# Kernel tuning notes

Hardware: AMD Instinct MI355X
Metric: run time of the kernel (lower is better)

Reference implementation:

```python
import jax, jax.numpy as jnp
import numpy as np

L, D, HID, NH, E, K, P, IMG, NC, B = 4, 384, 1536, 6, 8, 2, 16, 224, 1000, 8
S = (IMG // P) ** 2 + 1  # 197 tokens (cls + patches)
EPS = 1e-5


def setup_inputs() -> dict:
    ks = iter(jax.random.split(jax.random.key(0), 32))
    g = lambda shape, s=0.02: jax.random.normal(next(ks), shape, jnp.float32) * s
    pd = 3 * P * P
    return dict(
        x=jax.random.normal(next(ks), (B, 3, IMG, IMG), jnp.float32),
        patch_w=g((pd, D)), patch_b=g((D,)),
        cls_tok=g((1, 1, D)), pos=g((1, S, D)),
        qkv_w=g((L, D, 3 * D)), qkv_b=g((L, 3 * D)),
        proj_w=g((L, D, D)), proj_b=g((L, D)),
        ln1_g=jnp.ones((L, D)), ln1_b=jnp.zeros((L, D)),
        ln2_g=jnp.ones((L, D)), ln2_b=jnp.zeros((L, D)),
        router_w=g((L, D, E)), router_b=g((L, E)),
        w1=g((L, E, D, HID)), b1=g((L, E, HID)),
        w2=g((L, E, HID, D)), b2=g((L, E, D)),
        norm_g=jnp.ones((D,)), norm_b=jnp.zeros((D,)),
        fc_w=g((D, NC)), fc_b=g((NC,)),
    )


def _ln(x, g, b):
    m = x.mean(-1, keepdims=True)
    v = ((x - m) ** 2).mean(-1, keepdims=True)
    return (x - m) * jax.lax.rsqrt(v + EPS) * g + b


def _mha(x, wqkv, bqkv, wo, bo):
    Bx, Sx, Dx = x.shape
    hd = Dx // NH
    qkv = x @ wqkv + bqkv
    q, k, v = jnp.split(qkv, 3, axis=-1)
    q = q.reshape(Bx, Sx, NH, hd)
    k = k.reshape(Bx, Sx, NH, hd)
    v = v.reshape(Bx, Sx, NH, hd)
    att = jnp.einsum('bqhd,bkhd->bhqk', q, k) / jnp.sqrt(jnp.float32(hd))
    att = jax.nn.softmax(att, axis=-1)
    o = jnp.einsum('bhqk,bkhd->bqhd', att, v).reshape(Bx, Sx, Dx)
    return o @ wo + bo


def _moe(x, rw, rb, w1, b1, w2, b2, noise):
    # Faithful to the masked-dense SparseMoE: non-routed experts see zeros,
    # so occupied experts leak expert_j(0)=gelu(b1_j)@W2_j+b2_j to all tokens.
    xf = x.reshape(-1, x.shape[-1])                     # [T, D]
    logits = xf @ rw + rb + noise * 0.01                # noisy gating
    vals, idx = jax.lax.top_k(logits, K)                # [T, K]
    gates = jax.nn.softmax(vals, axis=-1)               # [T, K]
    h = jax.nn.gelu(jnp.einsum('td,edh->teh', xf, w1) + b1[None], approximate=False)
    y = jnp.einsum('teh,ehd->ted', h, w2) + b2[None]    # [T, E, D]
    bias0 = jnp.einsum('eh,ehd->ed', jax.nn.gelu(b1, approximate=False), w2) + b2  # expert_j(0)
    oh = jax.nn.one_hot(idx, E, dtype=xf.dtype)         # [T, K, E]
    occ = (oh.sum(0) > 0).astype(xf.dtype)              # [K, E] slot occupancy (mask.sum()>0)
    bias_sum = occ @ bias0                              # [K, D]
    y_sel = jnp.take_along_axis(y, idx[:, :, None], axis=1)  # [T, K, D]
    out = jnp.einsum('tk,tkd->td', gates, y_sel - bias0[idx] + bias_sum[None])
    return out.reshape(x.shape)


def reference(x, patch_w, patch_b, cls_tok, pos, qkv_w, qkv_b, proj_w, proj_b,
              ln1_g, ln1_b, ln2_g, ln2_b, router_w, router_b,
              w1, b1, w2, b2, norm_g, norm_b, fc_w, fc_b):
    Bx = x.shape[0]
    Hp = IMG // P
    # torch unfold patchify: (B,C,Hp,Wp,p,p) -> (B, N, C*p*p), channel-major features
    patches = x.reshape(Bx, 3, Hp, P, Hp, P).transpose(0, 2, 4, 1, 3, 5).reshape(Bx, Hp * Hp, 3 * P * P)
    t = patches @ patch_w + patch_b
    t = jnp.concatenate([jnp.broadcast_to(cls_tok, (Bx, 1, D)), t], axis=1) + pos
    nkey = jax.random.key(42)
    for l in range(L):
        a = _mha(t, qkv_w[l], qkv_b[l], proj_w[l], proj_b[l])
        t = _ln(t + a, ln1_g[l], ln1_b[l])
        noise = jax.random.normal(jax.random.fold_in(nkey, l), (Bx * S, E), t.dtype)
        m = _moe(t, router_w[l], router_b[l], w1[l], b1[l], w2[l], b2[l], noise)
        t = _ln(t + m, ln2_g[l], ln2_b[l])
    t = _ln(t, norm_g, norm_b)
    return t[:, 0] @ fc_w + fc_b
```

## Files before the change

### kernel.cpp

```cpp
#include <hip/hip_runtime.h>
#include <hip/hip_bf16.h>

constexpr int LYR  = 4;
constexpr int DM   = 384;
constexpr int HIDN = 1536;
constexpr int NHEAD = 6;
constexpr int HDIM = 64;
constexpr int NEXP = 8;
constexpr int SEQ  = 197;
constexpr int BATCH = 8;
constexpr int TOK  = BATCH * SEQ;
constexpr int NCLS = 1000;
constexpr int CAPE = TOK;
constexpr int NPATCH = BATCH * 196;
constexpr float EPSLN = 1e-5f;
constexpr int KP = 40;

typedef __attribute__((ext_vector_type(8))) short short8v;
typedef __attribute__((ext_vector_type(4))) float f32x4v;

__host__ __device__ inline void tf2x32(unsigned k0, unsigned k1, unsigned x0, unsigned x1,
                                       unsigned& y0, unsigned& y1) {
  unsigned ks2 = k0 ^ k1 ^ 0x1BD11BDAu;
  unsigned v0 = x0 + k0, v1 = x1 + k1;
#define TFR(r) { v0 += v1; v1 = (v1 << (r)) | (v1 >> (32 - (r))); v1 ^= v0; }
  TFR(13) TFR(15) TFR(26) TFR(6)
  v0 += k1;  v1 += ks2 + 1u;
  TFR(17) TFR(29) TFR(16) TFR(24)
  v0 += ks2; v1 += k0 + 2u;
  TFR(13) TFR(15) TFR(26) TFR(6)
  v0 += k0;  v1 += k1 + 3u;
  TFR(17) TFR(29) TFR(16) TFR(24)
  v0 += k1;  v1 += ks2 + 4u;
  TFR(13) TFR(15) TFR(26) TFR(6)
  v0 += ks2; v1 += k0 + 5u;
#undef TFR
  y0 = v0; y1 = v1;
}

__device__ inline float erfinv32(float x) {
  float w = -log1pf(-x * x);
  float p;
  if (w < 5.f) {
    w -= 2.5f;
    p = 2.81022636e-08f;
    p = fmaf(p, w, 3.43273939e-07f);
    p = fmaf(p, w, -3.5233877e-06f);
    p = fmaf(p, w, -4.39150654e-06f);
    p = fmaf(p, w, 0.00021858087f);
    p = fmaf(p, w, -0.00125372503f);
    p = fmaf(p, w, -0.00417768164f);
    p = fmaf(p, w, 0.246640727f);
    p = fmaf(p, w, 1.50140941f);
  } else {
    w = sqrtf(w) - 3.f;
    p = -0.000200214257f;
    p = fmaf(p, w, 0.000100950558f);
    p = fmaf(p, w, 0.00134934322f);
    p = fmaf(p, w, -0.00367342844f);
    p = fmaf(p, w, 0.00573950773f);
    p = fmaf(p, w, -0.0076224613f);
    p = fmaf(p, w, 0.00943887047f);
    p = fmaf(p, w, 1.00167406f);
    p = fmaf(p, w, 2.83297682f);
  }
  return p * x;
}

__device__ inline float gelu_f(float x) {
  return 0.5f * x * (1.f + erff(x * 0.70710678118654752f));
}

__device__ inline unsigned short bf16_rne(float x) {
  unsigned u = __float_as_uint(x);
  unsigned r = (u + 0x7fffu + ((u >> 16) & 1u)) >> 16;
  return (unsigned short)r;
}
__device__ inline void split2(float x, short& hs, short& ls) {
  unsigned hu = bf16_rne(x);
  float hf = __uint_as_float(hu << 16);
  unsigned lu = bf16_rne(x - hf);
  hs = (short)hu; ls = (short)lu;
}

__global__ __launch_bounds__(256) void convw_kernel(const float* __restrict__ src,
                                                    short* __restrict__ dst,
                                                    int K, int N) {
  const int nchunks = (K >> 5) * (N >> 4);
  const int chunk = blockIdx.x * 4 + (threadIdx.x >> 6);
  if (chunk >= nchunks) return;
  const int lane = threadIdx.x & 63;
  const long eoffS = (long)blockIdx.y * K * N;
  const long eoffD = (long)blockIdx.y * nchunks * 1024;
  const int nc = N >> 4;
  const int kt = chunk / nc, nt = chunk - kt * nc;
  const int n = nt * 16 + (lane & 15);
  const int kb = kt * 32 + (lane >> 4) * 8;
  short8v hv, lv;
#pragma unroll
  for (int j = 0; j < 8; j++) {
    short h, l;
    split2(src[eoffS + (long)(kb + j) * N + n], h, l);
    hv[j] = h; lv[j] = l;
  }
  *(short8v*)&dst[eoffD + (long)chunk * 1024 + lane * 8] = hv;
  *(short8v*)&dst[eoffD + (long)chunk * 1024 + 512 + lane * 8] = lv;
}

template <int KTOT, int NTOT, int MODE>
__global__ __launch_bounds__(256) void mfma_gemm_kernel(const float* __restrict__ A,
                                                        const short* __restrict__ Wf,
                                                        const float* __restrict__ bias,
                                                        const int* __restrict__ lists,
                                                        const int* __restrict__ counts,
                                                        float* __restrict__ out) {
  const int e = MODE ? blockIdx.y : 0;
  int rowsM;
  if (MODE) {
    const int n = counts[e];
    if ((int)blockIdx.x * 64 >= n) return;
    rowsM = min(64, n - (int)blockIdx.x * 64);
  } else {
    rowsM = min(64, TOK - (int)blockIdx.x * 64);
  }
  const int c0 = blockIdx.z * 64;
  const int tid = threadIdx.x;
  const int w = tid >> 6, lane = tid & 63;
  __shared__ int ent[64];
  __shared__ short xh[64 * KP];
  __shared__ short xl[64 * KP];
  if (MODE) {
    if (tid < 64) ent[tid] = (tid < rowsM) ? lists[e * CAPE + blockIdx.x * 64 + tid] : -1;
    __syncthreads();
  }
  const int sr = tid >> 2, skq = (tid & 3) * 8;
  bool okr; long arow = 0;
  if (MODE == 0) {
    okr = (sr < rowsM);
    arow = (long)(blockIdx.x * 64 + sr) * KTOT;
  } else {
    const int pid = ent[sr];
    okr = (pid >= 0);
    arow = (long)((MODE == 1) ? (pid >> 1) : pid) * KTOT;
  }
  const short* W = Wf + (long)e * (KTOT >> 5) * (NTOT >> 4) * 1024;
  const int wm = (w >> 1) * 32, wn = (w & 1) * 32;
  f32x4v Cr[2][2] = {};
  float4 ra = make_float4(0.f, 0.f, 0.f, 0.f), rb = ra;
  if (okr) {
    ra = *(const float4*)&A[arow + skq];
    rb = *(const float4*)&A[arow + skq + 4];
  }
  for (int kt = 0; kt < KTOT / 32; ++kt) {
    __syncthreads();
    {
      const float v[8] = {ra.x, ra.y, ra.z, ra.w, rb.x, rb.y, rb.z, rb.w};
      short8v hv, lv;
#pragma unroll
      for (int j = 0; j < 8; j++) { short h, l; split2(v[j], h, l); hv[j] = h; lv[j] = l; }
      *(short8v*)&xh[sr * KP + skq] = hv;
      *(short8v*)&xl[sr * KP + skq] = lv;
    }
    if (kt + 1 < KTOT / 32 && okr) {
      ra = *(const float4*)&A[arow + (kt + 1) * 32 + skq];
      rb = *(const float4*)&A[arow + (kt + 1) * 32 + skq + 4];
    }
    __syncthreads();
    short8v bhv[2], blv[2];
#pragma unroll
    for (int tt = 0; tt < 2; ++tt) {
      const int trow = wm + tt * 16 + (lane & 15);
      bhv[tt] = *(const short8v*)&xh[trow * KP + (lane >> 4) * 8];
      blv[tt] = *(const short8v*)&xl[trow * KP + (lane >> 4) * 8];
    }
    const long wkb = ((long)kt * (NTOT >> 4) + (c0 >> 4) + (wn >> 4)) * 1024;
#pragma unroll
    for (int nt = 0; nt < 2; ++nt) {
      const short8v wh = *(const short8v*)&W[wkb + nt * 1024 + lane * 8];
      const short8v wl = *(const short8v*)&W[wkb + nt * 1024 + 512 + lane * 8];
#pragma unroll
      for (int tt = 0; tt < 2; ++tt) {
        Cr[tt][nt] = __builtin_amdgcn_mfma_f32_16x16x32_bf16(wh, bhv[tt], Cr[tt][nt], 0, 0, 0);
        Cr[tt][nt] = __builtin_amdgcn_mfma_f32_16x16x32_bf16(wh, blv[tt], Cr[tt][nt], 0, 0, 0);
        Cr[tt][nt] = __builtin_amdgcn_mfma_f32_16x16x32_bf16(wl, bhv[tt], Cr[tt][nt], 0, 0, 0);
      }
    }
  }
  const int tl = lane & 15;
  const int nq = (lane >> 4) * 4;
#pragma unroll
  for (int tt = 0; tt < 2; ++tt) {
    const int trow = wm + tt * 16 + tl;
    if (trow < rowsM) {
      long orow;
      if (MODE == 0) orow = (long)(blockIdx.x * 64 + trow) * NTOT;
      else orow = (long)ent[trow] * NTOT;
#pragma unroll
      for (int nt = 0; nt < 2; ++nt) {
        const int n = c0 + wn + nt * 16 + nq;
        const float4 bv = *(const float4*)&bias[(MODE ? e * NTOT : 0) + n];
        float4 o;
        o.x = Cr[tt][nt][0] + bv.x;
        o.y = Cr[tt][nt][1] + bv.y;
        o.z = Cr[tt][nt][2] + bv.z;
        o.w = Cr[tt][nt][3] + bv.w;
        if (MODE == 1) { o.x = gelu_f(o.x); o.y = gelu_f(o.y); o.z = gelu_f(o.z); o.w = gelu_f(o.w); }
        *(float4*)&out[orow + n] = o;
      }
    }
  }
}

__global__ __launch_bounds__(256) void patch_mfma_kernel(const float* __restrict__ x,
                                                         const short* __restrict__ Wf,
                                                         const float* __restrict__ pb,
                                                         const float* __restrict__ pos,
                                                         float* __restrict__ t) {
  constexpr int KTOT = 768, NTOT = DM;
  const int rowsM = min(64, NPATCH - (int)blockIdx.x * 64);
  const int c0 = blockIdx.z * 64;
  const int tid = threadIdx.x;
  const int w = tid >> 6, lane = tid & 63;
  __shared__ short xh[64 * KP];
  __shared__ short xl[64 * KP];
  const int sr = tid >> 2, skq = (tid & 3) * 8;
  const bool okr = (sr < rowsM);
  const int p = blockIdx.x * 64 + sr;
  const int pbat = okr ? (p / 196) : 0;
  const int pn = okr ? (p - pbat * 196) : 0;
  const int hp = pn / 14, wp = pn - hp * 14;
  const float* xbase = x + ((long)pbat * 3 * 224 + hp * 16) * 224 + wp * 16;
  const int wm = (w >> 1) * 32, wn = (w & 1) * 32;
  f32x4v Cr[2][2] = {};
  float4 ra = make_float4(0.f, 0.f, 0.f, 0.f), rb = ra;
  if (okr) {
    const int f = skq;
    const int c = f >> 8, py = (f >> 4) & 15, px = f & 15;
    const float* ptr = xbase + ((long)c * 224 + py) * 224 + px;
    ra = *(const float4*)ptr;
    rb = *(const float4*)(ptr + 4);
  }
  for (int kt = 0; kt < KTOT / 32; ++kt) {
    __syncthreads();
    {
      const float v[8] = {ra.x, ra.y, ra.z, ra.w, rb.x, rb.y, rb.z, rb.w};
      short8v hv, lv;
#pragma unroll
      for (int j = 0; j < 8; j++) { short h, l; split2(v[j], h, l); hv[j] = h; lv[j] = l; }
      *(short8v*)&xh[sr * KP + skq] = hv;
      *(short8v*)&xl[sr * KP + skq] = lv;
    }
    if (kt + 1 < KTOT / 32 && okr) {
      const int f = (kt + 1) * 32 + skq;
      const int c = f >> 8, py = (f >> 4) & 15, px = f & 15;
      const float* ptr = xbase + ((long)c * 224 + py) * 224 + px;
      ra = *(const float4*)ptr;
      rb = *(const float4*)(ptr + 4);
    }
    __syncthreads();
    short8v bhv[2], blv[2];
#pragma unroll
    for (int tt = 0; tt < 2; ++tt) {
      const int trow = wm + tt * 16 + (lane & 15);
      bhv[tt] = *(const short8v*)&xh[trow * KP + (lane >> 4) * 8];
      blv[tt] = *(const short8v*)&xl[trow * KP + (lane >> 4) * 8];
    }
    const long wkb = ((long)kt * (NTOT >> 4) + (c0 >> 4) + (wn >> 4)) * 1024;
#pragma unroll
    for (int nt = 0; nt < 2; ++nt) {
      const short8v wh = *(const short8v*)&Wf[wkb + nt * 1024 + lane * 8];
      const short8v wl = *(const short8v*)&Wf[wkb + nt * 1024 + 512 + lane * 8];
#pragma unroll
      for (int tt = 0; tt < 2; ++tt) {
        Cr[tt][nt] = __builtin_amdgcn_mfma_f32_16x16x32_bf16(wh, bhv[tt], Cr[tt][nt], 0, 0, 0);
        Cr[tt][nt] = __builtin_amdgcn_mfma_f32_16x16x32_bf16(wh, blv[tt], Cr[tt][nt], 0, 0, 0);
        Cr[tt][nt] = __builtin_amdgcn_mfma_f32_16x16x32_bf16(wl, bhv[tt], Cr[tt][nt], 0, 0, 0);
      }
    }
  }
  const int tl = lane & 15;
  const int nq = (lane >> 4) * 4;
#pragma unroll
  for (int tt = 0; tt < 2; ++tt) {
    const int trow = wm + tt * 16 + tl;
    if (trow < rowsM) {
      const int r = blockIdx.x * 64 + trow;
      const int b2 = r / 196, n2 = r - b2 * 196;
      const long orow = (long)(b2 * SEQ + 1 + n2) * DM;
#pragma unroll
      for (int nt = 0; nt < 2; ++nt) {
        const int n = c0 + wn + nt * 16 + nq;
        const float4 bv = *(const float4*)&pb[n];
        const float4 pv = *(const float4*)&pos[(1 + n2) * DM + n];
        float4 o;
        o.x = Cr[tt][nt][0] + bv.x + pv.x;
        o.y = Cr[tt][nt][1] + bv.y + pv.y;
        o.z = Cr[tt][nt][2] + bv.z + pv.z;
        o.w = Cr[tt][nt][3] + bv.w + pv.w;
        *(float4*)&t[orow + n] = o;
      }
    }
  }
}

__global__ void cls_pos_kernel(const float* __restrict__ cls, const float* __restrict__ pos,
                               float* __restrict__ t) {
  int b = blockIdx.x, d = threadIdx.x;
  t[(b * SEQ) * DM + d] = cls[d] + pos[d];
}

constexpr int QT = 32;
constexpr int SP = 208;
__global__ __launch_bounds__(256) void attn_tile_kernel(const float* __restrict__ qkv,
                                                        float* __restrict__ out) {
  const int bh = blockIdx.x;
  const int b = bh / NHEAD, h = bh % NHEAD;
  const int q0 = blockIdx.y * QT;
  const int nq = min(QT, SEQ - q0);
  __shared__ float Qs[64][QT + 4];
  __shared__ float KV[64][68];
  __shared__ float Ss[QT][SP];
  const int tid = threadIdx.x;
  const int tx = tid & 15, ty = tid >> 4;
  for (int i = tid; i < QT * 16; i += 256) {
    const int q = i >> 4, dq = (i & 15) << 2;
    float4 v = make_float4(0.f, 0.f, 0.f, 0.f);
    if (q < nq) v = *(const float4*)&qkv[(long)(b * SEQ + q0 + q) * 1152 + h * HDIM + dq];
    Qs[dq + 0][q] = v.x; Qs[dq + 1][q] = v.y; Qs[dq + 2][q] = v.z; Qs[dq + 3][q] = v.w;
  }
  for (int kt = 0; kt < 4; ++kt) {
    const int kbase = kt * 64;
    __syncthreads();
    for (int i = tid; i < 64 * 16; i += 256) {
      const int key = i >> 4, dq = (i & 15) << 2;
      float4 v = make_float4(0.f, 0.f, 0.f, 0.f);
      if (kbase + key < SEQ)
        v = *(const float4*)&qkv[(long)(b * SEQ + kbase + key) * 1152 + DM + h * HDIM + dq];
      KV[dq + 0][key] = v.x; KV[dq + 1][key] = v.y; KV[dq + 2][key] = v.z; KV[dq + 3][key] = v.w;
    }
    __syncthreads();
    float acc[2][4] = {};
#pragma unroll 16
    for (int d = 0; d < 64; ++d) {
      const float4 k4 = *(const float4*)&KV[d][tx << 2];
      const float a0 = Qs[d][ty * 2], a1 = Qs[d][ty * 2 + 1];
      const float kk[4] = {k4.x, k4.y, k4.z, k4.w};
#pragma unroll
      for (int j = 0; j < 4; j++) {
        acc[0][j] = fmaf(a0, kk[j], acc[0][j]);
        acc[1][j] = fmaf(a1, kk[j], acc[1][j]);
      }
    }
#pragma unroll
    for (int i = 0; i < 2; i++) {
      float4 o = make_float4(acc[i][0] * 0.125f, acc[i][1] * 0.125f,
                             acc[i][2] * 0.125f, acc[i][3] * 0.125f);
      *(float4*)&Ss[ty * 2 + i][kbase + (tx << 2)] = o;
    }
  }
  __syncthreads();
  {
    const int row = tid >> 3, c = tid & 7;
    float m = -1e30f;
    for (int k = c; k < SEQ; k += 8) m = fmaxf(m, Ss[row][k]);
    m = fmaxf(m, __shfl_xor(m, 1)); m = fmaxf(m, __shfl_xor(m, 2)); m = fmaxf(m, __shfl_xor(m, 4));
    float s = 0.f;
    for (int k = c; k < SEQ; k += 8) { float e2 = __expf(Ss[row][k] - m); Ss[row][k] = e2; s += e2; }
    s += __shfl_xor(s, 1); s += __shfl_xor(s, 2); s += __shfl_xor(s, 4);
    const float inv = 1.f / s;
    for (int k = c; k < SEQ; k += 8) Ss[row][k] *= inv;
  }
  float acc[2][4] = {};
  for (int kt = 0; kt < 4; ++kt) {
    const int kbase = kt * 64;
    const int kend = min(64, SEQ - kbase);
    __syncthreads();
    for (int i = tid; i < 64 * 16; i += 256) {
      const int key = i >> 4, dq = (i & 15) << 2;
      float4 v = make_float4(0.f, 0.f, 0.f, 0.f);
      if (kbase + key < SEQ)
        v = *(const float4*)&qkv[(long)(b * SEQ + kbase + key) * 1152 + 2 * DM + h * HDIM + dq];
      *(float4*)&KV[key][dq] = v;
    }
    __syncthreads();
    for (int k = 0; k < kend; ++k) {
      const float4 v4 = *(const float4*)&KV[k][tx << 2];
      const float p0 = Ss[ty * 2][kbase + k], p1 = Ss[ty * 2 + 1][kbase + k];
      const float vv[4] = {v4.x, v4.y, v4.z, v4.w};
#pragma unroll
      for (int j = 0; j < 4; j++) {
        acc[0][j] = fmaf(p0, vv[j], acc[0][j]);
        acc[1][j] = fmaf(p1, vv[j], acc[1][j]);
      }
    }
  }
#pragma unroll
  for (int i = 0; i < 2; i++) {
    const int row = ty * 2 + i;
    if (row < nq) {
      float4 o = make_float4(acc[i][0], acc[i][1], acc[i][2], acc[i][3]);
      *(float4*)&out[(long)(b * SEQ + q0 + row) * DM + h * HDIM + (tx << 2)] = o;
    }
  }
}

__global__ __launch_bounds__(384) void add_ln_kernel(float* __restrict__ t,
                                                     const float* __restrict__ delta,
                                                     const float* __restrict__ g,
                                                     const float* __restrict__ bta) {
  int tok = blockIdx.x, d = threadIdx.x;
  float v = t[tok * DM + d] + delta[tok * DM + d];
  float sv = v, sq = v * v;
  for (int off = 32; off > 0; off >>= 1) { sv += __shfl_xor(sv, off); sq += __shfl_xor(sq, off); }
  __shared__ float rs[6], rq[6];
  int w = d >> 6, ln = d & 63;
  if (ln == 0) { rs[w] = sv; rq[w] = sq; }
  __syncthreads();
  float mean = 0.f, ms = 0.f;
#pragma unroll
  for (int i = 0; i < 6; i++) { mean += rs[i]; ms += rq[i]; }
  mean *= (1.f / DM); ms *= (1.f / DM);
  float inv = rsqrtf(ms - mean * mean + EPSLN);
  t[tok * DM + d] = (v - mean) * inv * g[d] + bta[d];
}

__global__ __launch_bounds__(256) void router_logits_kernel(const float* __restrict__ t,
                                                            const float* __restrict__ rw,
                                                            const float* __restrict__ rb,
                                                            unsigned k0, unsigned k1,
                                                            float* __restrict__ gates,
                                                            int* __restrict__ idxb) {
  const int tok = blockIdx.x * 4 + (threadIdx.x >> 6);
  const int lane = threadIdx.x & 63;
  const int e = lane & 7, j = lane >> 3;
  const float* xr = t + tok * DM;
  float acc = 0.f;
  for (int d2 = j * 48; d2 < j * 48 + 48; d2++) acc += xr[d2] * rw[d2 * NEXP + e];
  acc += __shfl_xor(acc, 8);
  acc += __shfl_xor(acc, 16);
  acc += __shfl_xor(acc, 32);
  if (lane < 8) {
    acc += rb[e];
    unsigned i = (unsigned)(tok * NEXP + e);
    unsigned y0, y1;
    tf2x32(k0, k1, 0u, i, y0, y1);
    unsigned bits = y0 ^ y1;
    float f = __uint_as_float(0x3f800000u | (bits >> 9)) - 1.0f;
    const float lo = -0.99999994f;
    float u = f * 2.0f + lo;
    u = fmaxf(lo, u);
    acc += 0.01f * (1.41421356f * erfinv32(u));
  }
  float lg[8];
#pragma unroll
  for (int qq = 0; qq < 8; qq++) lg[qq] = __shfl(acc, qq);
  if (lane == 0) {
    int i0 = 0; float v0 = lg[0];
#pragma unroll
    for (int qq = 1; qq < 8; qq++) if (lg[qq] > v0) { v0 = lg[qq]; i0 = qq; }
    int i1 = -1; float v1 = -1e30f;
#pragma unroll
    for (int qq = 0; qq < 8; qq++) if (qq != i0 && lg[qq] > v1) { v1 = lg[qq]; i1 = qq; }
    float e1 = __expf(v1 - v0);
    float g0 = 1.f / (1.f + e1);
    idxb[tok * 2] = i0; idxb[tok * 2 + 1] = i1;
    gates[tok * 2] = g0; gates[tok * 2 + 1] = 1.f - g0;
  }
}

__global__ __launch_bounds__(1024) void bucket_kernel(const int* __restrict__ idxb,
                                                      int* __restrict__ lists,
                                                      int* __restrict__ counts,
                                                      int* __restrict__ occ) {
  __shared__ int lc[NEXP];
  __shared__ int locc[2 * NEXP];
  const int tid = threadIdx.x;
  if (tid < NEXP) lc[tid] = 0;
  if (tid < 2 * NEXP) locc[tid] = 0;
  __syncthreads();
  for (int i = tid; i < 2 * TOK; i += 1024) {
    const int e = idxb[i];
    const int p = atomicAdd(&lc[e], 1);
    lists[e * CAPE + p] = i;
    locc[(i & 1) * NEXP + e] = 1;
  }
  __syncthreads();
  if (tid < NEXP) counts[tid] = lc[tid];
  if (tid < 2 * NEXP) occ[tid] = locc[tid];
}

__global__ void prep_kernel(const float* __restrict__ b2, float* __restrict__ bias0) {
  int e = blockIdx.x, c = threadIdx.x;
  bias0[e * DM + c] = b2[e * DM + c];
}

__global__ __launch_bounds__(384) void bias0_partial_kernel(const float* __restrict__ b1,
                                                            const float* __restrict__ w2,
                                                            float* __restrict__ bias0) {
  const int e = blockIdx.x, kc = blockIdx.y;
  __shared__ float gb[128];
  const int tid = threadIdx.x;
  if (tid < 128) gb[tid] = gelu_f(b1[e * HIDN + kc * 128 + tid]);
  __syncthreads();
  float acc = 0.f;
  const float* W = w2 + ((long)e * HIDN + kc * 128) * DM + tid;
  for (int j2 = 0; j2 < 128; j2++) acc += gb[j2] * W[(long)j2 * DM];
  atomicAdd(&bias0[e * DM + tid], acc);
}

__global__ __launch_bounds__(384) void bias_sum_kernel(const float* __restrict__ bias0,
                                                       const int* __restrict__ occ,
                                                       float* __restrict__ bias_sum) {
  int k = blockIdx.x, d = threadIdx.x;
  float acc = 0.f;
#pragma unroll
  for (int e = 0; e < NEXP; e++)
    if (occ[k * NEXP + e]) acc += bias0[e * DM + d];
  bias_sum[k * DM + d] = acc;
}

__global__ __launch_bounds__(384) void moe_combine_ln_kernel(float* __restrict__ t,
                                                             const float* __restrict__ ybuf,
                                                             const float* __restrict__ gates,
                                                             const int* __restrict__ idxb,
                                                             const float* __restrict__ bias0,
                                                             const float* __restrict__ bias_sum,
                                                             const float* __restrict__ g,
                                                             const float* __restrict__ bta) {
  int tok = blockIdx.x, d = threadIdx.x;
  float g0 = gates[tok * 2], g1 = gates[tok * 2 + 1];
  int i0 = idxb[tok * 2], i1 = idxb[tok * 2 + 1];
  float m0 = ybuf[(tok * 2) * DM + d] - bias0[i0 * DM + d] + bias_sum[d];
  float m1 = ybuf[(tok * 2 + 1) * DM + d] - bias0[i1 * DM + d] + bias_sum[DM + d];
  float v = t[tok * DM + d] + g0 * m0 + g1 * m1;
  float sv = v, sq = v * v;
  for (int off = 32; off > 0; off >>= 1) { sv += __shfl_xor(sv, off); sq += __shfl_xor(sq, off); }
  __shared__ float rs[6], rq[6];
  int w = d >> 6, ln = d & 63;
  if (ln == 0) { rs[w] = sv; rq[w] = sq; }
  __syncthreads();
  float mean = 0.f, ms = 0.f;
#pragma unroll
  for (int i = 0; i < 6; i++) { mean += rs[i]; ms += rq[i]; }
  mean *= (1.f / DM); ms *= (1.f / DM);
  float inv = rsqrtf(ms - mean * mean + EPSLN);
  t[tok * DM + d] = (v - mean) * inv * g[d] + bta[d];
}

__global__ __launch_bounds__(256) void final_kernel(const float* __restrict__ t,
                                                    const float* __restrict__ ng,
                                                    const float* __restrict__ nb,
                                                    const float* __restrict__ fw,
                                                    const float* __restrict__ fb,
                                                    float* __restrict__ out) {
  int b = blockIdx.x, chunk = blockIdx.y, tid = threadIdx.x;
  __shared__ float xr[DM];
  __shared__ float rs[4], rq[4];
  const float* row = t + (b * SEQ) * DM;
  float sv = 0.f, sq = 0.f;
  for (int i = tid; i < DM; i += 256) { float x = row[i]; xr[i] = x; sv += x; sq += x * x; }
  for (int off = 32; off > 0; off >>= 1) { sv += __shfl_xor(sv, off); sq += __shfl_xor(sq, off); }
  int w = tid >> 6, ln = tid & 63;
  if (ln == 0) { rs[w] = sv; rq[w] = sq; }
  __syncthreads();
  float mean = (rs[0] + rs[1] + rs[2] + rs[3]) * (1.f / DM);
  float ms = (rq[0] + rq[1] + rq[2] + rq[3]) * (1.f / DM);
  float inv = rsqrtf(ms - mean * mean + EPSLN);
  for (int i = tid; i < DM; i += 256) xr[i] = (xr[i] - mean) * inv * ng[i] + nb[i];
  __syncthreads();
  int c = chunk * 250 + tid;
  if (tid < 250) {
    float acc = fb[c];
    for (int k = 0; k < DM; k++) acc += xr[k] * fw[k * NCLS + c];
    out[b * NCLS + c] = acc;
  }
}

extern "C" void kernel_launch(void* const* d_in, const int* in_sizes, int n_in,
                              void* d_out, int out_size, void* d_ws, size_t ws_size,
                              hipStream_t stream) {
  const float* x       = (const float*)d_in[0];
  const float* patch_w = (const float*)d_in[1];
  const float* patch_b = (const float*)d_in[2];
  const float* cls_tok = (const float*)d_in[3];
  const float* pos     = (const float*)d_in[4];
  const float* qkv_w   = (const float*)d_in[5];
  const float* qkv_b   = (const float*)d_in[6];
  const float* proj_w  = (const float*)d_in[7];
  const float* proj_b  = (const float*)d_in[8];
  const float* ln1_g   = (const float*)d_in[9];
  const float* ln1_b   = (const float*)d_in[10];
  const float* ln2_g   = (const float*)d_in[11];
  const float* ln2_b   = (const float*)d_in[12];
  const float* router_w = (const float*)d_in[13];
  const float* router_b = (const float*)d_in[14];
  const float* w1      = (const float*)d_in[15];
  const float* b1      = (const float*)d_in[16];
  const float* w2      = (const float*)d_in[17];
  const float* b2      = (const float*)d_in[18];
  const float* norm_g  = (const float*)d_in[19];
  const float* norm_b  = (const float*)d_in[20];
  const float* fc_w    = (const float*)d_in[21];
  const float* fc_b    = (const float*)d_in[22];

  float* ws = (float*)d_ws;
  float* t        = ws;
  float* qkv      = t + TOK * DM;
  float* attn     = qkv + TOK * 1152;
  float* proj     = attn + TOK * DM;
  float* ybuf     = proj + TOK * DM;
  float* bias0    = ybuf + TOK * 2 * DM;
  float* bias_sum = bias0 + NEXP * DM;
  float* gates    = bias_sum + 2 * DM;
  int* idxb   = (int*)(gates + TOK * 2);
  int* lists  = idxb + TOK * 2;
  int* counts = lists + NEXP * CAPE;
  int* occ    = counts + NEXP;
  float* hbuf = (float*)(occ + 2 * NEXP);
  short* wqf  = (short*)(hbuf + 2 * TOK * HIDN);
  short* wpf  = wqf + 864 * 1024;
  short* w1f  = wpf + 288 * 1024;
  short* w2f  = w1f + 8 * 1152 * 1024;
  short* wpatf = w2f + 8 * 1152 * 1024;

  convw_kernel<<<dim3(144, 1), 256, 0, stream>>>(patch_w, wpatf, 768, DM);
  patch_mfma_kernel<<<dim3(25, 1, 6), 256, 0, stream>>>(x, wpatf, patch_b, pos, t);
  cls_pos_kernel<<<BATCH, DM, 0, stream>>>(cls_tok, pos, t);

  for (int l = 0; l < LYR; l++) {
    convw_kernel<<<dim3(216, 1), 256, 0, stream>>>(qkv_w + (long)l * DM * 1152, wqf, DM, 1152);
    convw_kernel<<<dim3(72, 1), 256, 0, stream>>>(proj_w + (long)l * DM * DM, wpf, DM, DM);
    convw_kernel<<<dim3(288, NEXP), 256, 0, stream>>>(w1 + (long)l * NEXP * DM * HIDN, w1f, DM, HIDN);
    convw_kernel<<<dim3(288, NEXP), 256, 0, stream>>>(w2 + (long)l * NEXP * HIDN * DM, w2f, HIDN, DM);

    mfma_gemm_kernel<DM, 1152, 0><<<dim3(25, 1, 18), 256, 0, stream>>>(
        t, wqf, qkv_b + l * 1152, nullptr, nullptr, qkv);
    attn_tile_kernel<<<dim3(BATCH * NHEAD, 7), 256, 0, stream>>>(qkv, attn);
    mfma_gemm_kernel<DM, DM, 0><<<dim3(25, 1, 6), 256, 0, stream>>>(
        attn, wpf, proj_b + l * DM, nullptr, nullptr, proj);
    add_ln_kernel<<<TOK, DM, 0, stream>>>(t, proj, ln1_g + l * DM, ln1_b + l * DM);

    prep_kernel<<<NEXP, DM, 0, stream>>>(b2 + l * NEXP * DM, bias0);
    bias0_partial_kernel<<<dim3(NEXP, 12), 384, 0, stream>>>(
        b1 + l * NEXP * HIDN, w2 + (long)l * NEXP * HIDN * DM, bias0);
    unsigned kl0, kl1;
    tf2x32(0u, 42u, 0u, (unsigned)l, kl0, kl1);
    router_logits_kernel<<<TOK / 4, 256, 0, stream>>>(
        t, router_w + l * DM * NEXP, router_b + l * NEXP, kl0, kl1, gates, idxb);
    bucket_kernel<<<1, 1024, 0, stream>>>(idxb, lists, counts, occ);
    bias_sum_kernel<<<2, 384, 0, stream>>>(bias0, occ, bias_sum);
    mfma_gemm_kernel<DM, HIDN, 1><<<dim3(25, NEXP, 24), 256, 0, stream>>>(
        t, w1f, b1 + l * NEXP * HIDN, lists, counts, hbuf);
    mfma_gemm_kernel<HIDN, DM, 2><<<dim3(25, NEXP, 6), 256, 0, stream>>>(
        hbuf, w2f, b2 + l * NEXP * DM, lists, counts, ybuf);
    moe_combine_ln_kernel<<<TOK, DM, 0, stream>>>(t, ybuf, gates, idxb, bias0, bias_sum,
                                                  ln2_g + l * DM, ln2_b + l * DM);
  }

  final_kernel<<<dim3(BATCH, 4), 256, 0, stream>>>(t, norm_g, norm_b, fc_w, fc_b,
                                                   (float*)d_out);
}
```

Baseline: 913.7 us.

## Pre-split activations into bf16 hi/lo planes in producers; GEMMs load fragments directly

Producer kernels (patch embed, cls, attention, add-LN, combine-LN, expert FFN1 epilogue) now also write activations as bf16 hi/lo split planes. The GEMMs read these straight from global memory into MFMA fragments, dropping the per-tile LDS staging, the in-loop fp32 split and both barriers. The grid is also reordered so column strips come first, which may improve weight reuse in cache. In exchange the producers write extra short buffers, and A-fragment loads are uncoalesced direct global reads.

```diff
diff --git a/kernel.cpp b/kernel.cpp
--- a/kernel.cpp
+++ b/kernel.cpp
@@ -17,6 +17,7 @@
 constexpr int KP = 40;
 
 typedef __attribute__((ext_vector_type(8))) short short8v;
+typedef __attribute__((ext_vector_type(4))) short short4v;
 typedef __attribute__((ext_vector_type(4))) float f32x4v;
 
 __host__ __device__ inline void tf2x32(unsigned k0, unsigned k1, unsigned x0, unsigned x1,
@@ -108,70 +109,47 @@
 }
 
 template <int KTOT, int NTOT, int MODE>
-__global__ __launch_bounds__(256) void mfma_gemm_kernel(const float* __restrict__ A,
-                                                        const short* __restrict__ Wf,
-                                                        const float* __restrict__ bias,
-                                                        const int* __restrict__ lists,
-                                                        const int* __restrict__ counts,
-                                                        float* __restrict__ out) {
-  const int e = MODE ? blockIdx.y : 0;
-  int rowsM;
-  if (MODE) {
-    const int n = counts[e];
-    if ((int)blockIdx.x * 64 >= n) return;
-    rowsM = min(64, n - (int)blockIdx.x * 64);
-  } else {
-    rowsM = min(64, TOK - (int)blockIdx.x * 64);
-  }
-  const int c0 = blockIdx.z * 64;
+__global__ __launch_bounds__(256) void gemm_frag_kernel(
+    const short* __restrict__ Ah, const short* __restrict__ Al,
+    const short* __restrict__ Wf, const float* __restrict__ bias,
+    const int* __restrict__ lists, const int* __restrict__ counts,
+    float* __restrict__ outF, short* __restrict__ outH, short* __restrict__ outL) {
+  constexpr int SPE = NTOT / 64;
+  const int strip = blockIdx.x;
+  const int e = MODE ? (strip / SPE) : 0;
+  const int c0 = (MODE ? (strip - e * SPE) : strip) * 64;
+  const int m = blockIdx.y;
+  int cnt = TOK;
+  if (MODE) cnt = counts[e];
+  if (m * 64 >= cnt) return;
   const int tid = threadIdx.x;
   const int w = tid >> 6, lane = tid & 63;
-  __shared__ int ent[64];
-  __shared__ short xh[64 * KP];
-  __shared__ short xl[64 * KP];
-  if (MODE) {
-    if (tid < 64) ent[tid] = (tid < rowsM) ? lists[e * CAPE + blockIdx.x * 64 + tid] : -1;
-    __syncthreads();
-  }
-  const int sr = tid >> 2, skq = (tid & 3) * 8;
-  bool okr; long arow = 0;
-  if (MODE == 0) {
-    okr = (sr < rowsM);
-    arow = (long)(blockIdx.x * 64 + sr) * KTOT;
-  } else {
-    const int pid = ent[sr];
-    okr = (pid >= 0);
-    arow = (long)((MODE == 1) ? (pid >> 1) : pid) * KTOT;
-  }
-  const short* W = Wf + (long)e * (KTOT >> 5) * (NTOT >> 4) * 1024;
   const int wm = (w >> 1) * 32, wn = (w & 1) * 32;
+  const int tl = lane & 15, kq = (lane >> 4) * 8;
+  int pid[2]; long arow[2];
+#pragma unroll
+  for (int tt = 0; tt < 2; ++tt) {
+    const int r = m * 64 + wm + tt * 16 + tl;
+    int p;
+    if (MODE) {
+      p = (r < cnt) ? lists[e * CAPE + r] : -1;
+      const int rr = (p < 0) ? 0 : ((MODE == 1) ? (p >> 1) : p);
+      arow[tt] = (long)rr * KTOT;
+    } else {
+      p = (r < TOK) ? r : -1;
+      arow[tt] = (long)((p < 0) ? 0 : r) * KTOT;
+    }
+    pid[tt] = p;
+  }
+  const short* W = Wf + (long)e * ((KTOT >> 5) * (NTOT >> 4)) * 1024;
   f32x4v Cr[2][2] = {};
-  float4 ra = make_float4(0.f, 0.f, 0.f, 0.f), rb = ra;
-  if (okr) {
-    ra = *(const float4*)&A[arow + skq];
-    rb = *(const float4*)&A[arow + skq + 4];
-  }
+#pragma unroll 4
   for (int kt = 0; kt < KTOT / 32; ++kt) {
-    __syncthreads();
-    {
-      const float v[8] = {ra.x, ra.y, ra.z, ra.w, rb.x, rb.y, rb.z, rb.w};
-      short8v hv, lv;
-#pragma unroll
-      for (int j = 0; j < 8; j++) { short h, l; split2(v[j], h, l); hv[j] = h; lv[j] = l; }
-      *(short8v*)&xh[sr * KP + skq] = hv;
-      *(short8v*)&xl[sr * KP + skq] = lv;
-    }
-    if (kt + 1 < KTOT / 32 && okr) {
-      ra = *(const float4*)&A[arow + (kt + 1) * 32 + skq];
-      rb = *(const float4*)&A[arow + (kt + 1) * 32 + skq + 4];
-    }
-    __syncthreads();
-    short8v bhv[2], blv[2];
+    short8v bh[2], bl[2];
 #pragma unroll
     for (int tt = 0; tt < 2; ++tt) {
-      const int trow = wm + tt * 16 + (lane & 15);
-      bhv[tt] = *(const short8v*)&xh[trow * KP + (lane >> 4) * 8];
-      blv[tt] = *(const short8v*)&xl[trow * KP + (lane >> 4) * 8];
+      bh[tt] = *(const short8v*)&Ah[arow[tt] + kt * 32 + kq];
+      bl[tt] = *(const short8v*)&Al[arow[tt] + kt * 32 + kq];
     }
     const long wkb = ((long)kt * (NTOT >> 4) + (c0 >> 4) + (wn >> 4)) * 1024;
 #pragma unroll
@@ -180,32 +158,34 @@
       const short8v wl = *(const short8v*)&W[wkb + nt * 1024 + 512 + lane * 8];
 #pragma unroll
       for (int tt = 0; tt < 2; ++tt) {
-        Cr[tt][nt] = __builtin_amdgcn_mfma_f32_16x16x32_bf16(wh, bhv[tt], Cr[tt][nt], 0, 0, 0);
-        Cr[tt][nt] = __builtin_amdgcn_mfma_f32_16x16x32_bf16(wh, blv[tt], Cr[tt][nt], 0, 0, 0);
-        Cr[tt][nt] = __builtin_amdgcn_mfma_f32_16x16x32_bf16(wl, bhv[tt], Cr[tt][nt], 0, 0, 0);
+        Cr[tt][nt] = __builtin_amdgcn_mfma_f32_16x16x32_bf16(wh, bh[tt], Cr[tt][nt], 0, 0, 0);
+        Cr[tt][nt] = __builtin_amdgcn_mfma_f32_16x16x32_bf16(wh, bl[tt], Cr[tt][nt], 0, 0, 0);
+        Cr[tt][nt] = __builtin_amdgcn_mfma_f32_16x16x32_bf16(wl, bh[tt], Cr[tt][nt], 0, 0, 0);
       }
     }
   }
-  const int tl = lane & 15;
   const int nq = (lane >> 4) * 4;
 #pragma unroll
   for (int tt = 0; tt < 2; ++tt) {
-    const int trow = wm + tt * 16 + tl;
-    if (trow < rowsM) {
-      long orow;
-      if (MODE == 0) orow = (long)(blockIdx.x * 64 + trow) * NTOT;
-      else orow = (long)ent[trow] * NTOT;
-#pragma unroll
-      for (int nt = 0; nt < 2; ++nt) {
-        const int n = c0 + wn + nt * 16 + nq;
-        const float4 bv = *(const float4*)&bias[(MODE ? e * NTOT : 0) + n];
-        float4 o;
-        o.x = Cr[tt][nt][0] + bv.x;
-        o.y = Cr[tt][nt][1] + bv.y;
-        o.z = Cr[tt][nt][2] + bv.z;
-        o.w = Cr[tt][nt][3] + bv.w;
-        if (MODE == 1) { o.x = gelu_f(o.x); o.y = gelu_f(o.y); o.z = gelu_f(o.z); o.w = gelu_f(o.w); }
-        *(float4*)&out[orow + n] = o;
+    if (pid[tt] < 0) continue;
+    const long orow = (long)pid[tt] * NTOT;
+#pragma unroll
+    for (int nt = 0; nt < 2; ++nt) {
+      const int n = c0 + wn + nt * 16 + nq;
+      const float4 bv = *(const float4*)&bias[(MODE ? e * NTOT : 0) + n];
+      float o0 = Cr[tt][nt][0] + bv.x, o1 = Cr[tt][nt][1] + bv.y;
+      float o2 = Cr[tt][nt][2] + bv.z, o3 = Cr[tt][nt][3] + bv.w;
+      if (MODE == 1) {
+        o0 = gelu_f(o0); o1 = gelu_f(o1); o2 = gelu_f(o2); o3 = gelu_f(o3);
+        short4v hv, lv; short hs, ls;
+        split2(o0, hs, ls); hv[0] = hs; lv[0] = ls;
+        split2(o1, hs, ls); hv[1] = hs; lv[1] = ls;
+        split2(o2, hs, ls); hv[2] = hs; lv[2] = ls;
+        split2(o3, hs, ls); hv[3] = hs; lv[3] = ls;
+        *(short4v*)&outH[orow + n] = hv;
+        *(short4v*)&outL[orow + n] = lv;
+      } else {
+        *(float4*)&outF[orow + n] = make_float4(o0, o1, o2, o3);
       }
     }
   }
@@ -215,7 +195,9 @@
                                                          const short* __restrict__ Wf,
                                                          const float* __restrict__ pb,
                                                          const float* __restrict__ pos,
-                                                         float* __restrict__ t) {
+                                                         float* __restrict__ t,
+                                                         short* __restrict__ tfh,
+                                                         short* __restrict__ tfl) {
   constexpr int KTOT = 768, NTOT = DM;
   const int rowsM = min(64, NPATCH - (int)blockIdx.x * 64);
   const int c0 = blockIdx.z * 64;
@@ -292,27 +274,39 @@
         const int n = c0 + wn + nt * 16 + nq;
         const float4 bv = *(const float4*)&pb[n];
         const float4 pv = *(const float4*)&pos[(1 + n2) * DM + n];
-        float4 o;
-        o.x = Cr[tt][nt][0] + bv.x + pv.x;
-        o.y = Cr[tt][nt][1] + bv.y + pv.y;
-        o.z = Cr[tt][nt][2] + bv.z + pv.z;
-        o.w = Cr[tt][nt][3] + bv.w + pv.w;
-        *(float4*)&t[orow + n] = o;
+        float o0 = Cr[tt][nt][0] + bv.x + pv.x;
+        float o1 = Cr[tt][nt][1] + bv.y + pv.y;
+        float o2 = Cr[tt][nt][2] + bv.z + pv.z;
+        float o3 = Cr[tt][nt][3] + bv.w + pv.w;
+        *(float4*)&t[orow + n] = make_float4(o0, o1, o2, o3);
+        short4v hv, lv; short hs, ls;
+        split2(o0, hs, ls); hv[0] = hs; lv[0] = ls;
+        split2(o1, hs, ls); hv[1] = hs; lv[1] = ls;
+        split2(o2, hs, ls); hv[2] = hs; lv[2] = ls;
+        split2(o3, hs, ls); hv[3] = hs; lv[3] = ls;
+        *(short4v*)&tfh[orow + n] = hv;
+        *(short4v*)&tfl[orow + n] = lv;
       }
     }
   }
 }
 
 __global__ void cls_pos_kernel(const float* __restrict__ cls, const float* __restrict__ pos,
-                               float* __restrict__ t) {
+                               float* __restrict__ t,
+                               short* __restrict__ tfh, short* __restrict__ tfl) {
   int b = blockIdx.x, d = threadIdx.x;
-  t[(b * SEQ) * DM + d] = cls[d] + pos[d];
+  float v = cls[d] + pos[d];
+  t[(b * SEQ) * DM + d] = v;
+  short hs, ls; split2(v, hs, ls);
+  tfh[(b * SEQ) * DM + d] = hs;
+  tfl[(b * SEQ) * DM + d] = ls;
 }
 
 constexpr int QT = 32;
 constexpr int SP = 208;
 __global__ __launch_bounds__(256) void attn_tile_kernel(const float* __restrict__ qkv,
-                                                        float* __restrict__ out) {
+                                                        short* __restrict__ afh,
+                                                        short* __restrict__ afl) {
   const int bh = blockIdx.x;
   const int b = bh / NHEAD, h = bh % NHEAD;
   const int q0 = blockIdx.y * QT;
@@ -398,8 +392,14 @@
   for (int i = 0; i < 2; i++) {
     const int row = ty * 2 + i;
     if (row < nq) {
-      float4 o = make_float4(acc[i][0], acc[i][1], acc[i][2], acc[i][3]);
-      *(float4*)&out[(long)(b * SEQ + q0 + row) * DM + h * HDIM + (tx << 2)] = o;
+      const long o = (long)(b * SEQ + q0 + row) * DM + h * HDIM + (tx << 2);
+      short4v hv, lv; short hs, ls;
+      split2(acc[i][0], hs, ls); hv[0] = hs; lv[0] = ls;
+      split2(acc[i][1], hs, ls); hv[1] = hs; lv[1] = ls;
+      split2(acc[i][2], hs, ls); hv[2] = hs; lv[2] = ls;
+      split2(acc[i][3], hs, ls); hv[3] = hs; lv[3] = ls;
+      *(short4v*)&afh[o] = hv;
+      *(short4v*)&afl[o] = lv;
     }
   }
 }
@@ -407,7 +407,9 @@
 __global__ __launch_bounds__(384) void add_ln_kernel(float* __restrict__ t,
                                                      const float* __restrict__ delta,
                                                      const float* __restrict__ g,
-                                                     const float* __restrict__ bta) {
+                                                     const float* __restrict__ bta,
+                                                     short* __restrict__ tfh,
+                                                     short* __restrict__ tfl) {
   int tok = blockIdx.x, d = threadIdx.x;
   float v = t[tok * DM + d] + delta[tok * DM + d];
   float sv = v, sq = v * v;
@@ -421,7 +423,11 @@
   for (int i = 0; i < 6; i++) { mean += rs[i]; ms += rq[i]; }
   mean *= (1.f / DM); ms *= (1.f / DM);
   float inv = rsqrtf(ms - mean * mean + EPSLN);
-  t[tok * DM + d] = (v - mean) * inv * g[d] + bta[d];
+  float y = (v - mean) * inv * g[d] + bta[d];
+  t[tok * DM + d] = y;
+  short hs, ls; split2(y, hs, ls);
+  tfh[tok * DM + d] = hs;
+  tfl[tok * DM + d] = ls;
 }
 
 __global__ __launch_bounds__(256) void router_logits_kernel(const float* __restrict__ t,
@@ -526,7 +532,9 @@
                                                              const float* __restrict__ bias0,
                                                              const float* __restrict__ bias_sum,
                                                              const float* __restrict__ g,
-                                                             const float* __restrict__ bta) {
+                                                             const float* __restrict__ bta,
+                                                             short* __restrict__ tfh,
+                                                             short* __restrict__ tfl) {
   int tok = blockIdx.x, d = threadIdx.x;
   float g0 = gates[tok * 2], g1 = gates[tok * 2 + 1];
   int i0 = idxb[tok * 2], i1 = idxb[tok * 2 + 1];
@@ -544,7 +552,11 @@
   for (int i = 0; i < 6; i++) { mean += rs[i]; ms += rq[i]; }
   mean *= (1.f / DM); ms *= (1.f / DM);
   float inv = rsqrtf(ms - mean * mean + EPSLN);
-  t[tok * DM + d] = (v - mean) * inv * g[d] + bta[d];
+  float y = (v - mean) * inv * g[d] + bta[d];
+  t[tok * DM + d] = y;
+  short hs, ls; split2(y, hs, ls);
+  tfh[tok * DM + d] = hs;
+  tfl[tok * DM + d] = ls;
 }
 
 __global__ __launch_bounds__(256) void final_kernel(const float* __restrict__ t,
@@ -606,8 +618,7 @@
   float* ws = (float*)d_ws;
   float* t        = ws;
   float* qkv      = t + TOK * DM;
-  float* attn     = qkv + TOK * 1152;
-  float* proj     = attn + TOK * DM;
+  float* proj     = qkv + TOK * 1152;
   float* ybuf     = proj + TOK * DM;
   float* bias0    = ybuf + TOK * 2 * DM;
   float* bias_sum = bias0 + NEXP * DM;
@@ -616,16 +627,21 @@
   int* lists  = idxb + TOK * 2;
   int* counts = lists + NEXP * CAPE;
   int* occ    = counts + NEXP;
-  float* hbuf = (float*)(occ + 2 * NEXP);
-  short* wqf  = (short*)(hbuf + 2 * TOK * HIDN);
-  short* wpf  = wqf + 864 * 1024;
-  short* w1f  = wpf + 288 * 1024;
-  short* w2f  = w1f + 8 * 1152 * 1024;
+  short* tfh = (short*)(occ + 2 * NEXP);
+  short* tfl = tfh + TOK * DM;
+  short* afh = tfl + TOK * DM;
+  short* afl = afh + TOK * DM;
+  short* hbh = afl + TOK * DM;
+  short* hbl = hbh + 2 * TOK * HIDN;
+  short* wqf = hbl + 2 * TOK * HIDN;
+  short* wpf = wqf + 864 * 1024;
+  short* w1f = wpf + 288 * 1024;
+  short* w2f = w1f + 8 * 1152 * 1024;
   short* wpatf = w2f + 8 * 1152 * 1024;
 
   convw_kernel<<<dim3(144, 1), 256, 0, stream>>>(patch_w, wpatf, 768, DM);
-  patch_mfma_kernel<<<dim3(25, 1, 6), 256, 0, stream>>>(x, wpatf, patch_b, pos, t);
-  cls_pos_kernel<<<BATCH, DM, 0, stream>>>(cls_tok, pos, t);
+  patch_mfma_kernel<<<dim3(25, 1, 6), 256, 0, stream>>>(x, wpatf, patch_b, pos, t, tfh, tfl);
+  cls_pos_kernel<<<BATCH, DM, 0, stream>>>(cls_tok, pos, t, tfh, tfl);
 
   for (int l = 0; l < LYR; l++) {
     convw_kernel<<<dim3(216, 1), 256, 0, stream>>>(qkv_w + (long)l * DM * 1152, wqf, DM, 1152);
@@ -633,12 +649,12 @@
     convw_kernel<<<dim3(288, NEXP), 256, 0, stream>>>(w1 + (long)l * NEXP * DM * HIDN, w1f, DM, HIDN);
     convw_kernel<<<dim3(288, NEXP), 256, 0, stream>>>(w2 + (long)l * NEXP * HIDN * DM, w2f, HIDN, DM);
 
-    mfma_gemm_kernel<DM, 1152, 0><<<dim3(25, 1, 18), 256, 0, stream>>>(
-        t, wqf, qkv_b + l * 1152, nullptr, nullptr, qkv);
-    attn_tile_kernel<<<dim3(BATCH * NHEAD, 7), 256, 0, stream>>>(qkv, attn);
-    mfma_gemm_kernel<DM, DM, 0><<<dim3(25, 1, 6), 256, 0, stream>>>(
-        attn, wpf, proj_b + l * DM, nullptr, nullptr, proj);
-    add_ln_kernel<<<TOK, DM, 0, stream>>>(t, proj, ln1_g + l * DM, ln1_b + l * DM);
+    gemm_frag_kernel<DM, 1152, 0><<<dim3(18, 25), 256, 0, stream>>>(
+        tfh, tfl, wqf, qkv_b + l * 1152, nullptr, nullptr, qkv, nullptr, nullptr);
+    attn_tile_kernel<<<dim3(BATCH * NHEAD, 7), 256, 0, stream>>>(qkv, afh, afl);
+    gemm_frag_kernel<DM, DM, 0><<<dim3(6, 25), 256, 0, stream>>>(
+        afh, afl, wpf, proj_b + l * DM, nullptr, nullptr, proj, nullptr, nullptr);
+    add_ln_kernel<<<TOK, DM, 0, stream>>>(t, proj, ln1_g + l * DM, ln1_b + l * DM, tfh, tfl);
 
     prep_kernel<<<NEXP, DM, 0, stream>>>(b2 + l * NEXP * DM, bias0);
     bias0_partial_kernel<<<dim3(NEXP, 12), 384, 0, stream>>>(
@@ -649,12 +665,12 @@
         t, router_w + l * DM * NEXP, router_b + l * NEXP, kl0, kl1, gates, idxb);
     bucket_kernel<<<1, 1024, 0, stream>>>(idxb, lists, counts, occ);
     bias_sum_kernel<<<2, 384, 0, stream>>>(bias0, occ, bias_sum);
-    mfma_gemm_kernel<DM, HIDN, 1><<<dim3(25, NEXP, 24), 256, 0, stream>>>(
-        t, w1f, b1 + l * NEXP * HIDN, lists, counts, hbuf);
-    mfma_gemm_kernel<HIDN, DM, 2><<<dim3(25, NEXP, 6), 256, 0, stream>>>(
-        hbuf, w2f, b2 + l * NEXP * DM, lists, counts, ybuf);
+    gemm_frag_kernel<DM, HIDN, 1><<<dim3(192, 25), 256, 0, stream>>>(
+        tfh, tfl, w1f, b1 + l * NEXP * HIDN, lists, counts, nullptr, hbh, hbl);
+    gemm_frag_kernel<HIDN, DM, 2><<<dim3(48, 25), 256, 0, stream>>>(
+        hbh, hbl, w2f, b2 + l * NEXP * DM, lists, counts, ybuf, nullptr, nullptr);
     moe_combine_ln_kernel<<<TOK, DM, 0, stream>>>(t, ybuf, gates, idxb, bias0, bias_sum,
-                                                  ln2_g + l * DM, ln2_b + l * DM);
+                                                  ln2_g + l * DM, ln2_b + l * DM, tfh, tfl);
   }
 
   final_kernel<<<dim3(BATCH, 4), 256, 0, stream>>>(t, norm_g, norm_b, fc_w, fc_b,
```

Measured after the change: 1.079 ms. 18.1% more time.
